# Performance work log

Measured on AMD Instinct MI355X. Metric: run time of the kernel, lower is better.

Reference implementation:

```python
import jax, jax.numpy as jnp
import numpy as np

N = 4096     # batch of positions
E = 32       # descriptor buckets (experts)
NBLK = 12    # residual blocks per head


def _ln(x, g, b, eps=1e-5):
    m = x.mean(-1, keepdims=True)
    v = ((x - m) ** 2).mean(-1, keepdims=True)
    return (x - m) / jnp.sqrt(v + eps) * g + b


def _gelu(x):
    return jax.nn.gelu(x, approximate=False)  # torch nn.GELU default = exact erf


def setup_inputs() -> dict:
    key = jax.random.key(0)
    ks = iter(jax.random.split(key, 64))

    def nrm(shape, scale=0.05):
        return jax.random.normal(next(ks), shape, jnp.float32) * scale

    return {
        "piece_idx": jax.random.randint(next(ks), (N, 64), 0, 12),
        "side_flag": jax.random.randint(next(ks), (N,), 0, 2),
        "ep_file": jax.random.randint(next(ks), (N,), 0, 8),
        "castle_ms": jax.random.uniform(next(ks), (N, 4), jnp.float32),
        "fifty_a": jax.random.uniform(next(ks), (N,), jnp.float32),
        "descriptor_index": jax.random.randint(next(ks), (N,), 0, E),
        # per-bucket embedding tables, stacked on a leading expert axis
        "Wp_w": nrm((E, 64, 12, 32)), "Wp_b": nrm((E, 64, 12, 32)),
        "Wc_w": nrm((E, 4, 32)), "Wc_b": nrm((E, 4, 32)),
        "Wep_w": nrm((E, 8, 32)), "Wep_b": nrm((E, 8, 32)),
        "Wf_w": nrm((E, 2, 32)), "Wf_b": nrm((E, 2, 32)),
        # per-bucket MLP head params (weights stored as [in,out])
        "fc1_w": nrm((E, 2240, 256)), "fc1_b": nrm((E, 256)),
        "ln1_g": jnp.ones((E, 256)), "ln1_b": jnp.zeros((E, 256)),
        "fc2_w": nrm((E, 256, 32)), "fc2_b": nrm((E, 32)),
        "ln2_g": jnp.ones((E, 32)), "ln2_b": jnp.zeros((E, 32)),
        "blkA_w": nrm((NBLK, E, 32, 32)), "blkA_b": nrm((NBLK, E, 32)),
        "blkA_g": jnp.ones((NBLK, E, 32)), "blkA_be": jnp.zeros((NBLK, E, 32)),
        "blkB_w": nrm((NBLK, E, 32, 32)), "blkB_b": nrm((NBLK, E, 32)),
        "blkB_g": jnp.ones((NBLK, E, 32)), "blkB_be": jnp.zeros((NBLK, E, 32)),
        "out_w": nrm((E, 32, 51)), "out_b": nrm((E, 51)),
        "bins": jnp.linspace(0.0, 1.0, 51),
    }


def reference(piece_idx, side_flag, ep_file, castle_ms, fifty_a, descriptor_index,
              Wp_w, Wp_b, Wc_w, Wc_b, Wep_w, Wep_b, Wf_w, Wf_b,
              fc1_w, fc1_b, ln1_g, ln1_b, fc2_w, fc2_b, ln2_g, ln2_b,
              blkA_w, blkA_b, blkA_g, blkA_be, blkB_w, blkB_b, blkB_g, blkB_be,
              out_w, out_b, bins):
    desc = descriptor_index
    side = side_flag.astype(bool)
    n = piece_idx.shape[0]

    # ---- per-bucket, side-selected embedding gathers -> x_emb [N,2240] ----
    sq = jnp.arange(64)
    pc = jnp.maximum(piece_idx, 0)                                 # clamp -1 -> 0
    w_emb = Wp_w[desc[:, None], sq[None, :], pc]                    # [N,64,32]
    b_emb = Wp_b[desc[:, None], sq[None, :], pc]
    piece_emb = jnp.where(side[:, None, None], b_emb, w_emb)
    piece_emb = piece_emb * (piece_idx >= 0)[..., None].astype(piece_emb.dtype)
    pieces_vec = piece_emb.reshape(n, 2048)

    Wc = jnp.where(side[:, None, None], Wc_b[desc], Wc_w[desc])     # [N,4,32]
    castle_vec = (castle_ms[..., None] * Wc).reshape(n, 128)

    Wep = jnp.where(side[:, None, None], Wep_b[desc], Wep_w[desc])  # [N,8,32]
    epc = jnp.maximum(ep_file, 0)
    ep_vec = jnp.take_along_axis(Wep, epc[:, None, None], axis=1)[:, 0]
    ep_vec = ep_vec * (ep_file >= 0)[:, None].astype(ep_vec.dtype)

    Wf = jnp.where(side[:, None, None], Wf_b[desc], Wf_w[desc])     # [N,2,32]
    fifty_vec = (1.0 - fifty_a)[:, None] * Wf[:, 0] + fifty_a[:, None] * Wf[:, 1]

    x = jnp.concatenate([pieces_vec, castle_vec, ep_vec, fifty_vec], axis=1)  # [N,2240]

    # ---- expert-routed dense layer: all-expert GEMM + per-token select ----
    def dense_moe(h, W, b):
        ha = jnp.einsum('nd,edh->neh', h, W)                        # [N,E,out]
        hsel = jnp.take_along_axis(ha, desc[:, None, None], axis=1)[:, 0]
        return hsel + b[desc]

    h = _ln(_gelu(dense_moe(x, fc1_w, fc1_b)), ln1_g[desc], ln1_b[desc])   # [N,256]
    h = _ln(_gelu(dense_moe(h, fc2_w, fc2_b)), ln2_g[desc], ln2_b[desc])   # [N,32]

    def blk(carry, p):
        wA, bA, gA, beA, wB, bB, gB, beB = p
        y = _ln(_gelu(dense_moe(carry, wA, bA)), gA[desc], beA[desc])
        y = _ln(_gelu(dense_moe(y, wB, bB)), gB[desc], beB[desc])
        return carry + y, None

    h, _ = jax.lax.scan(blk, h, (blkA_w, blkA_b, blkA_g, blkA_be,
                                 blkB_w, blkB_b, blkB_g, blkB_be))

    logits = dense_moe(_gelu(h), out_w, out_b)                      # [N,51]
    p_win = jnp.sum(jax.nn.softmax(logits, axis=-1) * bins, axis=-1, keepdims=True)
    return logits, p_win
```

## Files before the change

### kernel.cpp

```cpp
#include <hip/hip_runtime.h>
#include <math.h>

#define N 4096
#define E 32
#define NBLK 12
#define D_IN 2240
#define H1 256
#define H2 32
#define NOUT 51
#define MT 16
#define NPAD (N + E*(MT-1))
#define NTILE (NPAD/MT)
#define KSPLIT 4
#define NROWS 4608
#define GMAX 96

typedef short s8v __attribute__((ext_vector_type(8)));
typedef float f4v __attribute__((ext_vector_type(4)));

__device__ __forceinline__ float gelu(float x){
    return 0.5f * x * (1.0f + erff(x * 0.70710678118654752f));
}
__device__ __forceinline__ unsigned short f2bf(float f){
    unsigned int u = __float_as_uint(f);
    unsigned int r = (u + 0x7fffu + ((u >> 16) & 1u)) >> 16;
    return (unsigned short)r;
}
__device__ __forceinline__ float bflo(unsigned int u){ return __uint_as_float(u << 16); }
__device__ __forceinline__ float bfhi(unsigned int u){ return __uint_as_float(u & 0xffff0000u); }

template<int CTRL>
__device__ __forceinline__ float dppadd(float x){
    int y = __builtin_amdgcn_update_dpp(0, __float_as_int(x), CTRL, 0xF, 0xF, true);
    return x + __int_as_float(y);
}
__device__ __forceinline__ float red32(float x){
    x = dppadd<0x121>(x);
    x = dppadd<0x122>(x);
    x = dppadd<0x124>(x);
    x = dppadd<0x128>(x);
    int y = __builtin_amdgcn_ds_swizzle(__float_as_int(x), 0x401F);
    return x + __int_as_float(y);
}

__global__ void k_pack(const float* __restrict__ W2,
                       const float* __restrict__ Aw, const float* __restrict__ Bw,
                       unsigned int* __restrict__ w2pk_g, unsigned int* __restrict__ rpk_g){
    int j = blockIdx.x*256 + threadIdx.x;
    if (j < E*4096){
        int e = j >> 12, idx = j & 4095;
        int h = idx & 1, q = idx >> 1, cc = q & 31, p2 = q >> 5;
        int k0 = 4*p2 + 2*h;
        const float* W2e = W2 + (size_t)e*H1*H2;
        unsigned int lo = f2bf(W2e[k0*32 + cc]);
        unsigned int hi = f2bf(W2e[(k0+1)*32 + cc]);
        w2pk_g[((size_t)e << 12) + (p2*32 + cc)*2 + h] = lo | (hi << 16);
    } else {
        int i = j - E*4096;
        int slot = i & 511;
        int m = i >> 9;
        int e = m & 31, mat = m >> 5;
        int tb = mat >> 1, s = mat & 1;
        int h = slot & 1, q = slot >> 1, cc = q & 31, p2 = q >> 5;
        int k0 = 4*p2 + 2*h;
        const float* src = s ? Bw : Aw;
        size_t base = ((size_t)tb*E + e)*1024;
        unsigned int lo = f2bf(src[base + k0*32 + cc]);
        unsigned int hi = f2bf(src[base + (k0+1)*32 + cc]);
        rpk_g[((size_t)m << 9) + slot] = lo | (hi << 16);
    }
}

__global__ void k_prep(const int* __restrict__ piece_idx,
                       const int* __restrict__ side_flag,
                       const int* __restrict__ ep_file,
                       const float* __restrict__ castle_ms,
                       const float* __restrict__ fifty_a,
                       const int* __restrict__ desc_idx,
                       const float* __restrict__ Wp_w, const float* __restrict__ Wp_b,
                       const float* __restrict__ Wc_w, const float* __restrict__ Wc_b,
                       const float* __restrict__ Wep_w, const float* __restrict__ Wep_b,
                       const float* __restrict__ Wf_w, const float* __restrict__ Wf_b,
                       unsigned short* __restrict__ xs,
                       int* __restrict__ perm, int* __restrict__ tile_e,
                       int4* __restrict__ garr, int* __restrict__ ngroups){
    int tid = threadIdx.x;
    if (blockIdx.x == 0){
        __shared__ int scnt[E];
        __shared__ int spoff[E+1];
        __shared__ int scur[E];
        if (tid < E) scnt[tid] = 0;
        __syncthreads();
        for (int n = tid; n < N; n += blockDim.x) atomicAdd(&scnt[desc_idx[n]], 1);
        __syncthreads();
        if (tid == 0){
            int run = 0;
            for (int e = 0; e < E; e++){ spoff[e] = run; run += ((scnt[e] + MT - 1)/MT)*MT; }
            spoff[E] = run;
            int ng = 0;
            for (int e = 0; e < E; e++){
                int t0 = spoff[e]/MT, t1 = spoff[e+1]/MT;
                for (int t = t0; t < t1; t += 8){
                    int nv = t1 - t; if (nv > 8) nv = 8;
                    if (ng < GMAX) garr[ng] = make_int4(t, e, nv, 0);
                    ng++;
                }
            }
            *ngroups = (ng > GMAX) ? GMAX : ng;
        }
        __syncthreads();
        if (tid < E) scur[tid] = spoff[tid];
        for (int p = tid; p < NPAD + 64; p += blockDim.x) perm[p] = -1;
        __syncthreads();
        for (int n = tid; n < N; n += blockDim.x){
            int p = atomicAdd(&scur[desc_idx[n]], 1);
            perm[p] = n;
        }
        for (int t = tid; t < NTILE; t += blockDim.x){
            int p0 = t*MT;
            int e = -1;
            if (p0 < spoff[E]){
                for (int q = 0; q < E; q++){
                    if (p0 >= spoff[q] && p0 < spoff[q+1]){ e = q; break; }
                }
            }
            tile_e[t] = e;
        }
        s8v z = {0,0,0,0,0,0,0,0};
        for (int i = tid; i < D_IN/8; i += blockDim.x)
            *(s8v*)(xs + (size_t)N*D_IN + i*8) = z;
        return;
    }
    int row = blockIdx.x - 1;
    unsigned short* xr = xs + (size_t)row * D_IN;
    int d = desc_idx[row];
    int s = side_flag[row];
    __shared__ int pidx[64];
    if (tid < 64) pidx[tid] = piece_idx[row*64 + tid];
    __syncthreads();
    const float* Wp  = s ? Wp_b  : Wp_w;
    const float* Wc  = s ? Wc_b  : Wc_w;
    const float* Wep = s ? Wep_b : Wep_w;
    const float* Wf  = s ? Wf_b  : Wf_w;
    int ep  = ep_file[row];
    int epc = ep > 0 ? ep : 0;
    float a = fifty_a[row];
    for (int t = tid; t < D_IN/8; t += blockDim.x){
        int i0 = t*8;
        float v[8];
        if (i0 < 2048){
            int sq = i0 >> 5, c0 = i0 & 31;
            int pc = pidx[sq];
            float msk = pc >= 0 ? 1.0f : 0.0f;
            int pcc = pc > 0 ? pc : 0;
            const float* base = Wp + (((size_t)d*64 + sq)*12 + pcc)*32 + c0;
            float4 a0 = *(const float4*)base;
            float4 a1 = *(const float4*)(base + 4);
            v[0]=a0.x*msk; v[1]=a0.y*msk; v[2]=a0.z*msk; v[3]=a0.w*msk;
            v[4]=a1.x*msk; v[5]=a1.y*msk; v[6]=a1.z*msk; v[7]=a1.w*msk;
        } else if (i0 < 2176){
            int j = i0 - 2048; int ci = j >> 5, c0 = j & 31;
            float cv = castle_ms[row*4 + ci];
            const float* base = Wc + ((size_t)d*4 + ci)*32 + c0;
            float4 a0 = *(const float4*)base;
            float4 a1 = *(const float4*)(base + 4);
            v[0]=a0.x*cv; v[1]=a0.y*cv; v[2]=a0.z*cv; v[3]=a0.w*cv;
            v[4]=a1.x*cv; v[5]=a1.y*cv; v[6]=a1.z*cv; v[7]=a1.w*cv;
        } else if (i0 < 2208){
            int c0 = i0 - 2176;
            float msk = ep >= 0 ? 1.0f : 0.0f;
            const float* base = Wep + ((size_t)d*8 + epc)*32 + c0;
            float4 a0 = *(const float4*)base;
            float4 a1 = *(const float4*)(base + 4);
            v[0]=a0.x*msk; v[1]=a0.y*msk; v[2]=a0.z*msk; v[3]=a0.w*msk;
            v[4]=a1.x*msk; v[5]=a1.y*msk; v[6]=a1.z*msk; v[7]=a1.w*msk;
        } else {
            int c0 = i0 - 2208;
            #pragma unroll
            for (int j = 0; j < 8; j++)
                v[j] = (1.0f - a) * Wf[(size_t)d*64 + c0 + j] + a * Wf[(size_t)d*64 + 32 + c0 + j];
        }
        s8v p;
        #pragma unroll
        for (int j = 0; j < 8; j++) p[j] = (short)f2bf(v[j]);
        *(s8v*)(xr + i0) = p;
    }
}

__launch_bounds__(256)
__global__ void k_fc1(const int4* __restrict__ garr, const int* __restrict__ ngroups,
                      const unsigned short* __restrict__ xs,
                      const int* __restrict__ perm,
                      const float* __restrict__ W1,
                      float* __restrict__ h1p){
    int g = blockIdx.x;
    if (g >= *ngroups) return;
    int4 gi = garr[g];
    int tile0 = gi.x, e = gi.y, nv = gi.z;
    int kc = blockIdx.y, nh = blockIdx.z;
    int kstart = (kc <= 2) ? kc*18 : 53;
    int nsteps = (kc < 2) ? 18 : 17;
    int tid = threadIdx.x;
    int lane = tid & 63, wave = tid >> 6;
    int quad = lane >> 4, l16 = lane & 15;

    __shared__ float bst[32][133];

    const unsigned short* Arow[8];
    #pragma unroll
    for (int mt = 0; mt < 8; mt++){
        int p = perm[(tile0 + mt)*MT + l16];
        if (p < 0) p = N;
        Arow[mt] = xs + (size_t)p*D_IN + quad*8;
    }

    const float* Wb = W1 + (size_t)e*D_IN*H1 + nh*128;
    int kk0 = tid >> 5;
    int nq4 = (tid & 31) << 2;
    int cl0 = wave*32 + l16;
    int cl1 = cl0 + 16;

    f4v acc[8][2];
    #pragma unroll
    for (int mt = 0; mt < 8; mt++){ acc[mt][0] = (f4v){0.f,0.f,0.f,0.f}; acc[mt][1] = (f4v){0.f,0.f,0.f,0.f}; }

    int kend = kstart + nsteps;
    for (int s = kstart; s < kend; s++){
        int kb = s*32;
        #pragma unroll
        for (int p = 0; p < 4; p++){
            int kk = p*8 + kk0;
            float4 v = *(const float4*)(Wb + (size_t)(kb + kk)*H1 + nq4);
            bst[kk][nq4]   = v.x;
            bst[kk][nq4+1] = v.y;
            bst[kk][nq4+2] = v.z;
            bst[kk][nq4+3] = v.w;
        }
        __syncthreads();
        s8v b0, b1;
        #pragma unroll
        for (int j = 0; j < 8; j++){
            b0[j] = (short)f2bf(bst[quad*8 + j][cl0]);
            b1[j] = (short)f2bf(bst[quad*8 + j][cl1]);
        }
        #pragma unroll
        for (int mt = 0; mt < 8; mt++){
            s8v av = *(const s8v*)(Arow[mt] + kb);
            acc[mt][0] = __builtin_amdgcn_mfma_f32_16x16x32_bf16(av, b0, acc[mt][0], 0, 0, 0);
            acc[mt][1] = __builtin_amdgcn_mfma_f32_16x16x32_bf16(av, b1, acc[mt][1], 0, 0, 0);
        }
        __syncthreads();
    }
    int col0 = nh*128 + wave*32 + l16;
    float* out = h1p + (size_t)kc*NROWS*H1;
    #pragma unroll
    for (int mt = 0; mt < 8; mt++){
        if (mt >= nv) break;
        int posb = (tile0 + mt)*MT + quad*4;
        #pragma unroll
        for (int r = 0; r < 4; r++){
            out[(size_t)(posb + r)*H1 + col0]      = acc[mt][0][r];
            out[(size_t)(posb + r)*H1 + col0 + 16] = acc[mt][1][r];
        }
    }
}

__launch_bounds__(256)
__global__ void k_tail(const int* __restrict__ tile_e, const int* __restrict__ perm,
                       const float* __restrict__ h1p, const float* __restrict__ b1,
                       const float* __restrict__ g1, const float* __restrict__ be1,
                       const unsigned int* __restrict__ w2pk_g, const float* __restrict__ b2,
                       const float* __restrict__ g2, const float* __restrict__ be2,
                       const unsigned int* __restrict__ rpk,
                       const float* __restrict__ Abv, const float* __restrict__ Ag,
                       const float* __restrict__ Abe,
                       const float* __restrict__ Bb, const float* __restrict__ Bg,
                       const float* __restrict__ Bbe,
                       const float* __restrict__ Ow, const float* __restrict__ Ob,
                       const float* __restrict__ bins,
                       float* __restrict__ out){
    int th = blockIdx.x;
    int t  = th >> 1;
    int r0 = (th & 1) * 8;
    int e = tile_e[t];
    if (e < 0) return;
    int tid = threadIdx.x;

    __shared__ __align__(16) float        shf[8*260];
    __shared__ __align__(16) unsigned int W2pk[4096];
    __shared__ __align__(16) float        vecs[NBLK*6*32];
    __shared__ __align__(16) float        sh2[8][36];
    __shared__ __align__(16) float        sh3[8][36];

    {
        const unsigned int* src = w2pk_g + ((size_t)e << 12);
        for (int j = tid; j < 4096; j += 256) W2pk[j] = src[j];
    }
    for (int j = tid; j < NBLK*6*32; j += 256){
        int cc = j & 31, vi = (j >> 5) % 6, tb = j / 192;
        size_t wb = (size_t)tb*E + e;
        const float* src;
        switch(vi){ case 0: src=Abv; break; case 1: src=Ag; break; case 2: src=Abe; break;
                    case 3: src=Bb;  break; case 4: src=Bg; break; default: src=Bbe; }
        vecs[j] = src[wb*32 + cc];
    }
    #pragma unroll
    for (int it = 0; it < 2; it++){
        int slot = it*256 + tid;
        int r = slot >> 6, c4 = (slot & 63) << 2;
        int row = t*MT + r0 + r;
        float4 v = {0.f,0.f,0.f,0.f};
        #pragma unroll
        for (int kc = 0; kc < KSPLIT; kc++){
            float4 p = *(const float4*)(h1p + ((size_t)kc*NROWS + row)*H1 + c4);
            v.x += p.x; v.y += p.y; v.z += p.z; v.w += p.w;
        }
        float4 bb = *(const float4*)(b1 + e*H1 + c4);
        shf[r*260 + c4]   = gelu(v.x + bb.x);
        shf[r*260 + c4+1] = gelu(v.y + bb.y);
        shf[r*260 + c4+2] = gelu(v.z + bb.z);
        shf[r*260 + c4+3] = gelu(v.w + bb.w);
    }
    __syncthreads();

    int m = tid >> 5, c = tid & 31;
    {
        float s = 0.f, s2 = 0.f;
        #pragma unroll
        for (int j = 0; j < 8; j++){
            float x = shf[m*260 + c + 32*j];
            s += x; s2 += x*x;
        }
        s  = red32(s);
        s2 = red32(s2);
        float mean = s * (1.0f/H1);
        float var  = s2 * (1.0f/H1) - mean*mean;
        float rs = rsqrtf(var + 1e-5f);
        #pragma unroll
        for (int j = 0; j < 8; j++){
            int k = c + 32*j;
            shf[m*260 + k] = (shf[m*260 + k] - mean) * rs * g1[e*H1 + k] + be1[e*H1 + k];
        }
    }
    float hv;
    {
        const uint2* W2p = (const uint2*)W2pk;
        float q0=0.f,q1=0.f,q2=0.f,q3=0.f;
        #pragma unroll 8
        for (int p2 = 0; p2 < 64; p2++){
            uint2 w = W2p[p2*32 + c];
            float4 h4 = *(const float4*)(shf + m*260 + p2*4);
            q0 = fmaf(h4.x, bflo(w.x), q0);
            q1 = fmaf(h4.y, bfhi(w.x), q1);
            q2 = fmaf(h4.z, bflo(w.y), q2);
            q3 = fmaf(h4.w, bfhi(w.y), q3);
        }
        float acc = (q0+q1) + (q2+q3) + b2[e*H2 + c];
        float y = gelu(acc);
        float s  = red32(y);
        float s2 = red32(y*y);
        float mean2 = s * (1.0f/H2);
        float var2  = s2 * (1.0f/H2) - mean2*mean2;
        hv = (y - mean2) * rsqrtf(var2 + 1e-5f) * g2[e*H2+c] + be2[e*H2+c];
    }

    for (int tb = 0; tb < NBLK; tb++){
        const float* vA = &vecs[tb*192];
        const uint2* WA = (const uint2*)(rpk + (((size_t)(tb*2+0)*E + e) << 9));
        const uint2* WB = (const uint2*)(rpk + (((size_t)(tb*2+1)*E + e) << 9));
        sh2[m][c] = hv;
        float q0=0.f,q1=0.f,q2=0.f,q3=0.f;
        #pragma unroll
        for (int p2 = 0; p2 < 8; p2++){
            uint2 w = WA[p2*32 + c];
            float4 h4 = *(const float4*)(&sh2[m][p2*4]);
            q0 = fmaf(h4.x, bflo(w.x), q0);
            q1 = fmaf(h4.y, bfhi(w.x), q1);
            q2 = fmaf(h4.z, bflo(w.y), q2);
            q3 = fmaf(h4.w, bfhi(w.y), q3);
        }
        float ya = (q0+q1) + (q2+q3) + vA[c];
        ya = gelu(ya);
        float sa  = red32(ya);
        float sa2 = red32(ya*ya);
        float ma = sa * (1.0f/H2);
        float va = sa2 * (1.0f/H2) - ma*ma;
        float yA = (ya - ma) * rsqrtf(va + 1e-5f) * vA[32+c] + vA[64+c];
        sh3[m][c] = yA;
        q0=0.f; q1=0.f; q2=0.f; q3=0.f;
        #pragma unroll
        for (int p2 = 0; p2 < 8; p2++){
            uint2 w = WB[p2*32 + c];
            float4 h4 = *(const float4*)(&sh3[m][p2*4]);
            q0 = fmaf(h4.x, bflo(w.x), q0);
            q1 = fmaf(h4.y, bfhi(w.x), q1);
            q2 = fmaf(h4.z, bflo(w.y), q2);
            q3 = fmaf(h4.w, bfhi(w.y), q3);
        }
        float yb = (q0+q1) + (q2+q3) + vA[96+c];
        yb = gelu(yb);
        float sb  = red32(yb);
        float sb2 = red32(yb*yb);
        float mb = sb * (1.0f/H2);
        float vb = sb2 * (1.0f/H2) - mb*mb;
        hv += (yb - mb) * rsqrtf(vb + 1e-5f) * vA[128+c] + vA[160+c];
    }

    sh2[m][c] = gelu(hv);
    __syncthreads();
    int wave = tid >> 6, lane = tid & 63;
    const float* W = Ow + (size_t)e*32*NOUT;
    for (int rr = wave; rr < 8; rr += 4){
        int orow = perm[t*MT + r0 + rr];
        if (orow < 0) continue;
        float acc = (lane < NOUT) ? Ob[e*NOUT + lane] : -INFINITY;
        #pragma unroll
        for (int k = 0; k < 32; k++){
            float gk = sh2[rr][k];
            if (lane < NOUT) acc = fmaf(gk, W[k*NOUT + lane], acc);
        }
        if (lane < NOUT) out[(size_t)orow*NOUT + lane] = acc;
        float mx = acc;
        #pragma unroll
        for (int o = 32; o > 0; o >>= 1) mx = fmaxf(mx, __shfl_xor(mx, o));
        float pp = (lane < NOUT) ? expf(acc - mx) : 0.0f;
        float sum = pp;
        float pb = (lane < NOUT) ? pp * bins[lane] : 0.0f;
        float sb = pb;
        #pragma unroll
        for (int o = 32; o > 0; o >>= 1){ sum += __shfl_xor(sum, o); sb += __shfl_xor(sb, o); }
        if (lane == 0) out[(size_t)N*NOUT + orow] = sb / sum;
    }
}

extern "C" void kernel_launch(void* const* d_in, const int* in_sizes, int n_in,
                              void* d_out, int out_size, void* d_ws, size_t ws_size,
                              hipStream_t stream){
    const int*   piece_idx = (const int*)d_in[0];
    const int*   side_flag = (const int*)d_in[1];
    const int*   ep_file   = (const int*)d_in[2];
    const float* castle_ms = (const float*)d_in[3];
    const float* fifty_a   = (const float*)d_in[4];
    const int*   desc      = (const int*)d_in[5];
    const float* Wp_w  = (const float*)d_in[6];
    const float* Wp_b  = (const float*)d_in[7];
    const float* Wc_w  = (const float*)d_in[8];
    const float* Wc_b  = (const float*)d_in[9];
    const float* Wep_w = (const float*)d_in[10];
    const float* Wep_b = (const float*)d_in[11];
    const float* Wf_w  = (const float*)d_in[12];
    const float* Wf_b  = (const float*)d_in[13];
    const float* fc1_w = (const float*)d_in[14];
    const float* fc1_b = (const float*)d_in[15];
    const float* ln1_g = (const float*)d_in[16];
    const float* ln1_b = (const float*)d_in[17];
    const float* fc2_w = (const float*)d_in[18];
    const float* fc2_b = (const float*)d_in[19];
    const float* ln2_g = (const float*)d_in[20];
    const float* ln2_b = (const float*)d_in[21];
    const float* blkA_w  = (const float*)d_in[22];
    const float* blkA_b  = (const float*)d_in[23];
    const float* blkA_g  = (const float*)d_in[24];
    const float* blkA_be = (const float*)d_in[25];
    const float* blkB_w  = (const float*)d_in[26];
    const float* blkB_b  = (const float*)d_in[27];
    const float* blkB_g  = (const float*)d_in[28];
    const float* blkB_be = (const float*)d_in[29];
    const float* out_w = (const float*)d_in[30];
    const float* out_b = (const float*)d_in[31];
    const float* bins  = (const float*)d_in[32];

    char* wsp = (char*)d_ws;
    auto alloc = [&](size_t bytes){ void* p = (void*)wsp; wsp += (bytes + 255) & ~(size_t)255; return p; };
    int*            perm    = (int*)            alloc((size_t)(NPAD+128)*4);
    int*            tile_e  = (int*)            alloc((size_t)NTILE*4);
    int4*           garr    = (int4*)           alloc((size_t)GMAX*16);
    int*            ngroups = (int*)            alloc(256);
    unsigned int*   w2pk_g  = (unsigned int*)   alloc((size_t)E*4096*4);
    unsigned int*   rpk     = (unsigned int*)   alloc((size_t)24*E*512*4);
    unsigned short* xs      = (unsigned short*) alloc((size_t)(N+128)*D_IN*2);
    float*          h1p     = (float*)          alloc((size_t)KSPLIT*NROWS*H1*4);

    k_pack<<<2048, 256, 0, stream>>>(fc2_w, blkA_w, blkB_w, w2pk_g, rpk);
    k_prep<<<1 + N, 256, 0, stream>>>(piece_idx, side_flag, ep_file,
                                      castle_ms, fifty_a, desc,
                                      Wp_w, Wp_b, Wc_w, Wc_b,
                                      Wep_w, Wep_b, Wf_w, Wf_b,
                                      xs, perm, tile_e, garr, ngroups);
    k_fc1<<<dim3(GMAX, KSPLIT, 2), 256, 0, stream>>>(garr, ngroups, xs, perm, fc1_w, h1p);
    k_tail<<<NTILE*2, 256, 0, stream>>>(tile_e, perm, h1p, fc1_b, ln1_g, ln1_b,
                                        w2pk_g, fc2_b, ln2_g, ln2_b,
                                        rpk,
                                        blkA_b, blkA_g, blkA_be,
                                        blkB_b, blkB_g, blkB_be,
                                        out_w, out_b, bins, (float*)d_out);
}
```

Measured before the change: 280.9 us.

## Double-buffer fc1 weight tiles in LDS and split N into four 64-column slices

The fc1 grouped GEMM kernel now stages weight tiles through a two-slot LDS buffer, prefetching the next k-step into registers while the MFMAs for the current step run, which removes one barrier per step. The output width per block drops from 128 to 64 columns (grid z goes from 2 to 4), so each wave does one MFMA per m-tile instead of two. This doubles the block count for better occupancy and latency hiding, but the A tile loads from global memory are now repeated across twice as many blocks and each block does less MFMA work per barrier.

After: 315.5 us. 1.12x slower.

```diff
diff --git a/kernel.cpp b/kernel.cpp
--- a/kernel.cpp
+++ b/kernel.cpp
@@ -204,7 +204,7 @@
     int lane = tid & 63, wave = tid >> 6;
     int quad = lane >> 4, l16 = lane & 15;
 
-    __shared__ float bst[32][133];
+    __shared__ float bst[2][32][68];
 
     const unsigned short* Arow[8];
     #pragma unroll
@@ -214,44 +214,45 @@
         Arow[mt] = xs + (size_t)p*D_IN + quad*8;
     }
 
-    const float* Wb = W1 + (size_t)e*D_IN*H1 + nh*128;
-    int kk0 = tid >> 5;
-    int nq4 = (tid & 31) << 2;
-    int cl0 = wave*32 + l16;
-    int cl1 = cl0 + 16;
-
-    f4v acc[8][2];
+    const float* Wb = W1 + (size_t)e*D_IN*H1 + nh*64;
+    int kk_a = tid >> 4;
+    int kk_b = 16 + (tid >> 4);
+    int n4 = (tid & 15) << 2;
+    int cl = wave*16 + l16;
+
+    f4v acc[8];
     #pragma unroll
-    for (int mt = 0; mt < 8; mt++){ acc[mt][0] = (f4v){0.f,0.f,0.f,0.f}; acc[mt][1] = (f4v){0.f,0.f,0.f,0.f}; }
+    for (int mt = 0; mt < 8; mt++) acc[mt] = (f4v){0.f,0.f,0.f,0.f};
 
     int kend = kstart + nsteps;
+    float4 ra = *(const float4*)(Wb + (size_t)(kstart*32 + kk_a)*H1 + n4);
+    float4 rb = *(const float4*)(Wb + (size_t)(kstart*32 + kk_b)*H1 + n4);
+    *(float4*)&bst[0][kk_a][n4] = ra;
+    *(float4*)&bst[0][kk_b][n4] = rb;
+    __syncthreads();
+    int cur = 0;
     for (int s = kstart; s < kend; s++){
         int kb = s*32;
-        #pragma unroll
-        for (int p = 0; p < 4; p++){
-            int kk = p*8 + kk0;
-            float4 v = *(const float4*)(Wb + (size_t)(kb + kk)*H1 + nq4);
-            bst[kk][nq4]   = v.x;
-            bst[kk][nq4+1] = v.y;
-            bst[kk][nq4+2] = v.z;
-            bst[kk][nq4+3] = v.w;
-        }
-        __syncthreads();
-        s8v b0, b1;
-        #pragma unroll
-        for (int j = 0; j < 8; j++){
-            b0[j] = (short)f2bf(bst[quad*8 + j][cl0]);
-            b1[j] = (short)f2bf(bst[quad*8 + j][cl1]);
-        }
+        if (s + 1 < kend){
+            ra = *(const float4*)(Wb + (size_t)((s+1)*32 + kk_a)*H1 + n4);
+            rb = *(const float4*)(Wb + (size_t)((s+1)*32 + kk_b)*H1 + n4);
+        }
+        s8v b0;
+        #pragma unroll
+        for (int j = 0; j < 8; j++) b0[j] = (short)f2bf(bst[cur][quad*8 + j][cl]);
         #pragma unroll
         for (int mt = 0; mt < 8; mt++){
             s8v av = *(const s8v*)(Arow[mt] + kb);
-            acc[mt][0] = __builtin_amdgcn_mfma_f32_16x16x32_bf16(av, b0, acc[mt][0], 0, 0, 0);
-            acc[mt][1] = __builtin_amdgcn_mfma_f32_16x16x32_bf16(av, b1, acc[mt][1], 0, 0, 0);
+            acc[mt] = __builtin_amdgcn_mfma_f32_16x16x32_bf16(av, b0, acc[mt], 0, 0, 0);
+        }
+        if (s + 1 < kend){
+            *(float4*)&bst[cur^1][kk_a][n4] = ra;
+            *(float4*)&bst[cur^1][kk_b][n4] = rb;
         }
         __syncthreads();
-    }
-    int col0 = nh*128 + wave*32 + l16;
+        cur ^= 1;
+    }
+    int col0 = nh*64 + wave*16 + l16;
     float* out = h1p + (size_t)kc*NROWS*H1;
     #pragma unroll
     for (int mt = 0; mt < 8; mt++){
@@ -259,8 +260,7 @@
         int posb = (tile0 + mt)*MT + quad*4;
         #pragma unroll
         for (int r = 0; r < 4; r++){
-            out[(size_t)(posb + r)*H1 + col0]      = acc[mt][0][r];
-            out[(size_t)(posb + r)*H1 + col0 + 16] = acc[mt][1][r];
+            out[(size_t)(posb + r)*H1 + col0] = acc[mt][r];
         }
     }
 }
@@ -487,7 +487,7 @@
                                       Wp_w, Wp_b, Wc_w, Wc_b,
                                       Wep_w, Wep_b, Wf_w, Wf_b,
                                       xs, perm, tile_e, garr, ngroups);
-    k_fc1<<<dim3(GMAX, KSPLIT, 2), 256, 0, stream>>>(garr, ngroups, xs, perm, fc1_w, h1p);
+    k_fc1<<<dim3(GMAX, KSPLIT, 4), 256, 0, stream>>>(garr, ngroups, xs, perm, fc1_w, h1p);
     k_tail<<<NTILE*2, 256, 0, stream>>>(tile_e, perm, h1p, fc1_b, ln1_g, ln1_b,
                                         w2pk_g, fc2_b, ln2_g, ln2_b,
                                         rpk,
```
